# Kernel optimization log

Measured on AMD Instinct MI355X. Metric: run time of the kernel, lower is better.

## Reference

```python
import jax, jax.numpy as jnp
import numpy as np

N_NODES = 100000
NEG_SLOPE = 0.2


def gat_conv(x, W, att_src, att_dst, bias, src, dst, heads, out_ch):
    # x: [N, F_in]; W: [F_in, heads*out_ch]; att_*: [heads, out_ch]; bias: [heads*out_ch]
    N = x.shape[0]
    h = (x @ W).reshape(N, heads, out_ch)                 # [N, H, C]
    a_src = jnp.sum(h * att_src[None], axis=-1)           # [N, H]
    a_dst = jnp.sum(h * att_dst[None], axis=-1)           # [N, H]
    # per-edge unnormalized attention logits (PyG GATConv)
    alpha = jax.nn.leaky_relu(a_src[src] + a_dst[dst], NEG_SLOPE)   # [E, H]
    # scatter-softmax over edges grouped by destination node
    m = jax.ops.segment_max(alpha, dst, num_segments=N)   # [N, H]
    m = jnp.where(jnp.isfinite(m), m, 0.0)
    e = jnp.exp(alpha - m[dst])                           # [E, H]
    s = jax.ops.segment_sum(e, dst, num_segments=N)       # [N, H]
    alpha = e / (s[dst] + 1e-16)
    # weighted scatter-add aggregation of neighbor features
    out = jax.ops.segment_sum(alpha[:, :, None] * h[src], dst, num_segments=N)  # [N, H, C]
    return out.reshape(N, heads * out_ch) + bias


def setup_inputs() -> dict:
    key = jax.random.key(0)
    ks = jax.random.split(key, 10)
    F_in = 128
    x = jax.random.normal(ks[0], (N_NODES, F_in), dtype=jnp.float32)
    edge_index = jax.random.randint(ks[1], (2, 3200000), 0, N_NODES, dtype=jnp.int64)
    g = 0.1
    return {
        "x": x,
        "edge_index": edge_index,
        "W1": jax.random.normal(ks[2], (F_in, 32), jnp.float32) * g,
        "att_src1": jax.random.normal(ks[3], (2, 16), jnp.float32) * g,
        "att_dst1": jax.random.normal(ks[4], (2, 16), jnp.float32) * g,
        "b1": jnp.zeros((32,), jnp.float32),
        "W2": jax.random.normal(ks[5], (32, 2), jnp.float32) * g,
        "att_src2": jax.random.normal(ks[6], (1, 2), jnp.float32) * g,
        "att_dst2": jax.random.normal(ks[7], (1, 2), jnp.float32) * g,
        "b2": jnp.zeros((2,), jnp.float32),
    }


def reference(x, edge_index, W1, att_src1, att_dst1, b1, W2, att_src2, att_dst2, b2):
    N = x.shape[0]
    # add self-loops (PyG GATConv default add_self_loops=True)
    loops = jnp.arange(N, dtype=edge_index.dtype)
    src = jnp.concatenate([edge_index[0], loops])
    dst = jnp.concatenate([edge_index[1], loops])
    h = gat_conv(x, W1, att_src1, att_dst1, b1, src, dst, heads=2, out_ch=16)
    h = jax.nn.elu(h)
    h = gat_conv(h, W2, att_src2, att_dst2, b2, src, dst, heads=1, out_ch=2)
    return jax.nn.log_softmax(h, axis=1)
```

## Files before the change

kernel.cpp:

```cpp
#include <hip/hip_runtime.h>
#include <hip/hip_bf16.h>

#define LEAK  0.2f
#define NPB   200
#define CAP   8192
#define CAPSH 13
#define SBITS 17
#define SMASK 0x1FFFF
#define CHUNK 4096

__global__ __launch_bounds__(512) void kbin(const int* __restrict__ ei, int E, int K,
                                            int* __restrict__ cursor,
                                            int* __restrict__ binned) {
    __shared__ int hist[512], lo[512], gb[512], lc[512];
    __shared__ int2 stag[CHUNK];
    __shared__ int probe;
    int t = threadIdx.x;
    hist[t] = 0;
    if (t == 0) probe = 0;
    __syncthreads();
    if (t < 256) {
        int zc = 0;
#pragma unroll
        for (int j = 0; j < 4; j++) zc += (ei[(t * 4 + j) * 2 + 1] == 0) ? 1 : 0;
        if (zc) atomicAdd(&probe, zc);
    }
    __syncthreads();
    int f = (probe == 1024);
    int e0 = blockIdx.x * CHUNK;
    int ss[8], dd[8];
#pragma unroll
    for (int i = 0; i < 8; i++) {
        int e = e0 + t + 512 * i;
        ss[i] = -1;
        dd[i] = 0;
        if (e < E) {
            int s, d;
            if (f) { s = ei[2 * (long long)e]; d = ei[2 * ((long long)e + E)]; }
            else   { s = ei[e];                d = ei[(long long)e + E]; }
            ss[i] = s;
            dd[i] = d;
            atomicAdd(&hist[d / NPB], 1);
        }
    }
    __syncthreads();
    int v = hist[t], x = v;
    for (int o = 1; o < 512; o <<= 1) {
        int y = (t >= o) ? hist[t - o] : 0;
        __syncthreads();
        x += y;
        hist[t] = x;
        __syncthreads();
    }
    int tb = x - v;
    lo[t] = tb;
    lc[t] = tb;
    if (t < K && v) {
        int rel = atomicAdd(&cursor[t], v);
        gb[t] = (t << CAPSH) + rel;
    }
    __syncthreads();
#pragma unroll
    for (int i = 0; i < 8; i++) {
        if (ss[i] >= 0) {
            int bk = dd[i] / NPB;
            int pos = atomicAdd(&lc[bk], 1);
            stag[pos] = make_int2(ss[i], dd[i]);
        }
    }
    __syncthreads();
    int cnt = min(CHUNK, E - e0);
#pragma unroll
    for (int i = 0; i < 8; i++) {
        int idx = t + 512 * i;
        if (idx < cnt) {
            int2 sd2 = stag[idx];
            int bk = sd2.y / NPB;
            int dloc = sd2.y - bk * NPB;
            int gpos = gb[bk] + (idx - lo[bk]);
            if (gpos < ((bk + 1) << CAPSH))
                binned[gpos] = sd2.x | (dloc << SBITS);
        }
    }
}

__global__ __launch_bounds__(256) void k1(const float* __restrict__ x,
                                          const float* __restrict__ W1,
                                          const float* __restrict__ atts,
                                          const float* __restrict__ attd,
                                          float* __restrict__ h1,
                                          float* __restrict__ a1s,
                                          float* __restrict__ a1d, int N) {
    __shared__ float Ws[128 * 32];
    __shared__ float xs[64 * 132];
    int t = threadIdx.x;
    const float4* W4 = (const float4*)W1;
    float4* Ws4 = (float4*)Ws;
#pragma unroll
    for (int i = 0; i < 4; i++) Ws4[t + 256 * i] = W4[t + 256 * i];
    long long node0 = (long long)blockIdx.x * 64;
    const float4* x4 = (const float4*)x;
    float4* xs4 = (float4*)xs;
#pragma unroll
    for (int i = 0; i < 8; i++) {
        int idx = t + 256 * i;
        int row = idx >> 5, col = idx & 31;
        long long n = node0 + row;
        float4 v = make_float4(0.f, 0.f, 0.f, 0.f);
        if (n < N) v = x4[n * 32 + col];
        xs4[row * 33 + col] = v;
    }
    __syncthreads();

    int cg = t & 7, ns = t >> 3;
    const float4* xr0 = (const float4*)(xs + (ns * 2) * 132);
    const float4* xr1 = (const float4*)(xs + (ns * 2 + 1) * 132);
    float acc0[4] = {0.f, 0.f, 0.f, 0.f}, acc1[4] = {0.f, 0.f, 0.f, 0.f};
#pragma unroll 8
    for (int k4 = 0; k4 < 32; k4++) {
        float4 xa = xr0[k4], xb = xr1[k4];
        float av[4] = {xa.x, xa.y, xa.z, xa.w};
        float bv[4] = {xb.x, xb.y, xb.z, xb.w};
#pragma unroll
        for (int i = 0; i < 4; i++) {
            float4 w = Ws4[(k4 * 4 + i) * 8 + cg];
            acc0[0] = fmaf(av[i], w.x, acc0[0]);
            acc0[1] = fmaf(av[i], w.y, acc0[1]);
            acc0[2] = fmaf(av[i], w.z, acc0[2]);
            acc0[3] = fmaf(av[i], w.w, acc0[3]);
            acc1[0] = fmaf(bv[i], w.x, acc1[0]);
            acc1[1] = fmaf(bv[i], w.y, acc1[1]);
            acc1[2] = fmaf(bv[i], w.z, acc1[2]);
            acc1[3] = fmaf(bv[i], w.w, acc1[3]);
        }
    }
    long long gn0 = node0 + ns * 2, gn1 = gn0 + 1;
    float4* h14 = (float4*)h1;
    if (gn0 < N) h14[gn0 * 8 + cg] = make_float4(acc0[0], acc0[1], acc0[2], acc0[3]);
    if (gn1 < N) h14[gn1 * 8 + cg] = make_float4(acc1[0], acc1[1], acc1[2], acc1[3]);

    float ps0 = 0.f, pd0 = 0.f, ps1 = 0.f, pd1 = 0.f;
#pragma unroll
    for (int i = 0; i < 4; i++) {
        float aa = atts[cg * 4 + i], dd = attd[cg * 4 + i];
        ps0 = fmaf(acc0[i], aa, ps0);
        pd0 = fmaf(acc0[i], dd, pd0);
        ps1 = fmaf(acc1[i], aa, ps1);
        pd1 = fmaf(acc1[i], dd, pd1);
    }
#pragma unroll
    for (int m = 1; m < 4; m <<= 1) {
        ps0 += __shfl_xor(ps0, m, 64);
        pd0 += __shfl_xor(pd0, m, 64);
        ps1 += __shfl_xor(ps1, m, 64);
        pd1 += __shfl_xor(pd1, m, 64);
    }
    if ((cg & 3) == 0) {
        int hd = cg >> 2;
        if (gn0 < N) { a1s[gn0 * 2 + hd] = ps0; a1d[gn0 * 2 + hd] = pd0; }
        if (gn1 < N) { a1s[gn1 * 2 + hd] = ps1; a1d[gn1 * 2 + hd] = pd1; }
    }
}

__global__ __launch_bounds__(1024) void kfused(const int* __restrict__ cursor,
                                               const int* __restrict__ binned,
                                               const float* __restrict__ h1,
                                               const float* __restrict__ a1s,
                                               const float* __restrict__ a1d,
                                               const float* __restrict__ b1,
                                               const float* __restrict__ W2,
                                               const float* __restrict__ as2,
                                               const float* __restrict__ ad2,
                                               float4* __restrict__ pk,
                                               int* __restrict__ srcs,
                                               int* __restrict__ off,
                                               int* __restrict__ deg, int N) {
    __shared__ int lsrc[CAP];
    __shared__ int ldeg[NPB], lcur[NPB], loff[NPB];
    __shared__ int sd[1024];
    int b = blockIdx.x, t = threadIdx.x;
    int node0 = b * NPB;
    int nn = min(NPB, N - node0);
    int cnt = cursor[b];
    if (cnt > CAP) cnt = CAP;
    const int* bb = binned + ((long long)b << CAPSH);
    if (t < NPB) ldeg[t] = 0;
    __syncthreads();
    for (int i = t; i < cnt; i += 1024) atomicAdd(&ldeg[bb[i] >> SBITS], 1);
    __syncthreads();
    int v = (t < nn) ? ldeg[t] : 0, x = v;
    sd[t] = x;
    __syncthreads();
    for (int o = 1; o < 1024; o <<= 1) {
        int y = (t >= o) ? sd[t - o] : 0;
        __syncthreads();
        x += y;
        sd[t] = x;
        __syncthreads();
    }
    if (t < nn) {
        int rel = x - v;
        loff[t] = rel;
        lcur[t] = rel;
        off[node0 + t] = (b << CAPSH) + rel;
        deg[node0 + t] = v;
    }
    __syncthreads();
    for (int i = t; i < cnt; i += 1024) {
        int p = bb[i];
        int pos = atomicAdd(&lcur[p >> SBITS], 1);
        lsrc[pos] = p & SMASK;
    }
    __syncthreads();
    for (int i = t; i < cnt; i += 1024) srcs[((long long)b << CAPSH) + i] = lsrc[i];

    int wv = t >> 6, lane = t & 63;
    int e8 = lane >> 3, c4 = lane & 7, hd = c4 >> 2;
    bool wlane = (c4 & 3) == 0;
    const float4* h14 = (const float4*)h1;
    for (int ni = wv; ni < nn; ni += 16) {
        int n = node0 + ni;
        float a1dn = a1d[2 * n + hd];
        int base = loff[ni], g = ldeg[ni];
        float4 acc = make_float4(0.f, 0.f, 0.f, 0.f);
        float wsum = 0.f;
        for (int tt = e8 - 1; tt < g; tt += 8) {
            int s = (tt < 0) ? n : lsrc[base + tt];
            float al = a1s[2 * s + hd] + a1dn;
            al = al > 0.f ? al : LEAK * al;
            float w = __expf(al);
            float4 hv = h14[(size_t)s * 8 + c4];
            acc.x = fmaf(w, hv.x, acc.x);
            acc.y = fmaf(w, hv.y, acc.y);
            acc.z = fmaf(w, hv.z, acc.z);
            acc.w = fmaf(w, hv.w, acc.w);
            if (wlane) wsum += w;
        }
#pragma unroll
        for (int m = 8; m < 64; m <<= 1) {
            acc.x += __shfl_xor(acc.x, m, 64);
            acc.y += __shfl_xor(acc.y, m, 64);
            acc.z += __shfl_xor(acc.z, m, 64);
            acc.w += __shfl_xor(acc.w, m, 64);
            wsum += __shfl_xor(wsum, m, 64);
        }
        float wsH = __shfl(wsum, hd * 4, 64);
        float inv = 1.f / (wsH + 1e-16f);
        float4 bv = ((const float4*)b1)[c4];
        float4 t1;
        t1.x = acc.x * inv + bv.x;
        t1.y = acc.y * inv + bv.y;
        t1.z = acc.z * inv + bv.z;
        t1.w = acc.w * inv + bv.w;
        t1.x = t1.x > 0.f ? t1.x : __expf(t1.x) - 1.f;
        t1.y = t1.y > 0.f ? t1.y : __expf(t1.y) - 1.f;
        t1.z = t1.z > 0.f ? t1.z : __expf(t1.z) - 1.f;
        t1.w = t1.w > 0.f ? t1.w : __expf(t1.w) - 1.f;
        const float4* W24 = (const float4*)W2;
        float4 wA = W24[c4 * 2], wB = W24[c4 * 2 + 1];
        float p0 = t1.x * wA.x + t1.y * wA.z + t1.z * wB.x + t1.w * wB.z;
        float p1 = t1.x * wA.y + t1.y * wA.w + t1.z * wB.y + t1.w * wB.w;
#pragma unroll
        for (int m = 1; m < 8; m <<= 1) {
            p0 += __shfl_xor(p0, m, 64);
            p1 += __shfl_xor(p1, m, 64);
        }
        if (lane == 0)
            pk[n] = make_float4(p0 * as2[0] + p1 * as2[1], p0, p1,
                                p0 * ad2[0] + p1 * ad2[1]);
    }
}

__global__ __launch_bounds__(256) void kagg2(const int* __restrict__ off,
                                             const int* __restrict__ deg,
                                             const int* __restrict__ srcs,
                                             const float4* __restrict__ pk,
                                             const float* __restrict__ b2,
                                             float* __restrict__ out, int N) {
    int wv = threadIdx.x >> 6;
    int lane = threadIdx.x & 63;
    int n = blockIdx.x * 4 + wv;
    if (n >= N) return;
    float adn = pk[n].w;
    int base = off[n], g = deg[n];
    float a0 = 0.f, a1v = 0.f, ws = 0.f;
    for (int t = lane - 1; t < g; t += 64) {
        int s = (t < 0) ? n : srcs[base + t];
        float4 p = pk[s];
        float al = p.x + adn;
        al = al > 0.f ? al : LEAK * al;
        float w = __expf(al);
        a0 = fmaf(w, p.y, a0);
        a1v = fmaf(w, p.z, a1v);
        ws += w;
    }
#pragma unroll
    for (int m = 1; m < 64; m <<= 1) {
        a0 += __shfl_xor(a0, m, 64);
        a1v += __shfl_xor(a1v, m, 64);
        ws += __shfl_xor(ws, m, 64);
    }
    if (lane == 0) {
        float inv = 1.f / (ws + 1e-16f);
        float o0 = a0 * inv + b2[0];
        float o1 = a1v * inv + b2[1];
        float mx = fmaxf(o0, o1);
        float lse = mx + __logf(__expf(o0 - mx) + __expf(o1 - mx));
        out[2 * n] = o0 - lse;
        out[2 * n + 1] = o1 - lse;
    }
}

extern "C" void kernel_launch(void* const* d_in, const int* in_sizes, int n_in,
                              void* d_out, int out_size, void* d_ws, size_t ws_size,
                              hipStream_t stream) {
    const float* x   = (const float*)d_in[0];
    const int*   ei  = (const int*)d_in[1];
    const float* W1  = (const float*)d_in[2];
    const float* as1 = (const float*)d_in[3];
    const float* ad1 = (const float*)d_in[4];
    const float* b1  = (const float*)d_in[5];
    const float* W2  = (const float*)d_in[6];
    const float* as2 = (const float*)d_in[7];
    const float* ad2 = (const float*)d_in[8];
    const float* b2  = (const float*)d_in[9];
    float* out = (float*)d_out;

    int N = out_size / 2;
    int E = in_sizes[1] / 2;
    int K = (N + NPB - 1) / NPB;

    float* ws    = (float*)d_ws;
    float* h1    = ws;
    float4* pk   = (float4*)(h1 + (size_t)N * 32);
    float* a1s   = (float*)(pk + (size_t)N);
    float* a1d   = a1s + (size_t)N * 2;
    int* deg     = (int*)(a1d + (size_t)N * 2);
    int* off     = deg + N;
    int* srcs    = off + N;
    int* binned  = srcs + (size_t)K * CAP;
    int* cursor  = binned + (size_t)K * CAP;

    int nblkE = (E + CHUNK - 1) / CHUNK;

    hipMemsetAsync(cursor, 0, K * sizeof(int), stream);
    kbin<<<nblkE, 512, 0, stream>>>(ei, E, K, cursor, binned);
    k1<<<(N + 63) / 64, 256, 0, stream>>>(x, W1, as1, ad1, h1, a1s, a1d, N);
    kfused<<<K, 1024, 0, stream>>>(cursor, binned, h1, a1s, a1d,
                                   b1, W2, as2, ad2, pk, srcs, off, deg, N);
    kagg2<<<(N + 3) / 4, 256, 0, stream>>>(off, deg, srcs, pk, b2, out, N);
}
```

Measured before the change: 245.8 us.

## Store layer-1 features as fp16, simplify binning, pack offsets, half-wave agg2

Layer-1 hidden features are stored as packed fp16 instead of fp32, halving gather traffic in the fused aggregation. The edge binning kernel drops its shared-memory staging and block-wide scan, scattering directly with per-bucket atomics over larger chunks. The fused kernel keeps loaded edges in registers and replaces the 1024-wide shared-memory scan with a wave shuffle scan. Offset and degree are packed into one int. The second aggregation uses 32 lanes per node. The fp16 storage lowers precision, and the direct scatter writes less coalesced output.

```diff
diff --git a/kernel.cpp b/kernel.cpp
--- a/kernel.cpp
+++ b/kernel.cpp
@@ -1,19 +1,28 @@
 #include <hip/hip_runtime.h>
 #include <hip/hip_bf16.h>
-
-#define LEAK  0.2f
-#define NPB   200
-#define CAP   8192
-#define CAPSH 13
-#define SBITS 17
-#define SMASK 0x1FFFF
-#define CHUNK 4096
+#include <hip/hip_fp16.h>
+
+#define LEAK   0.2f
+#define NPB    200
+#define CAP    8192
+#define CAPSH  13
+#define SBITS  17
+#define SMASK  0x1FFFF
+#define CHUNKB 8192
+
+__device__ __forceinline__ unsigned pkh(float a, float b) {
+    __half2 h = __floats2half2_rn(a, b);
+    return *(unsigned*)&h;
+}
+__device__ __forceinline__ float2 uph(unsigned u) {
+    __half2 h = *(__half2*)&u;
+    return __half22float2(h);
+}
 
 __global__ __launch_bounds__(512) void kbin(const int* __restrict__ ei, int E, int K,
                                             int* __restrict__ cursor,
                                             int* __restrict__ binned) {
-    __shared__ int hist[512], lo[512], gb[512], lc[512];
-    __shared__ int2 stag[CHUNK];
+    __shared__ int hist[512], gb[512], lc[512];
     __shared__ int probe;
     int t = threadIdx.x;
     hist[t] = 0;
@@ -27,59 +36,36 @@
     }
     __syncthreads();
     int f = (probe == 1024);
-    int e0 = blockIdx.x * CHUNK;
-    int ss[8], dd[8];
-#pragma unroll
-    for (int i = 0; i < 8; i++) {
+    int e0 = blockIdx.x * CHUNKB;
+    int ss[16], dd[16];
+#pragma unroll
+    for (int i = 0; i < 16; i++) {
         int e = e0 + t + 512 * i;
         ss[i] = -1;
         dd[i] = 0;
         if (e < E) {
             int s, d;
-            if (f) { s = ei[2 * (long long)e]; d = ei[2 * ((long long)e + E)]; }
-            else   { s = ei[e];                d = ei[(long long)e + E]; }
+            if (f) { s = ei[2 * e]; d = ei[2 * (e + E)]; }
+            else   { s = ei[e];     d = ei[e + E]; }
             ss[i] = s;
             dd[i] = d;
             atomicAdd(&hist[d / NPB], 1);
         }
     }
     __syncthreads();
-    int v = hist[t], x = v;
-    for (int o = 1; o < 512; o <<= 1) {
-        int y = (t >= o) ? hist[t - o] : 0;
-        __syncthreads();
-        x += y;
-        hist[t] = x;
-        __syncthreads();
-    }
-    int tb = x - v;
-    lo[t] = tb;
-    lc[t] = tb;
-    if (t < K && v) {
-        int rel = atomicAdd(&cursor[t], v);
-        gb[t] = (t << CAPSH) + rel;
-    }
-    __syncthreads();
-#pragma unroll
-    for (int i = 0; i < 8; i++) {
+    int h = hist[t];
+    lc[t] = 0;
+    if (t < K && h) gb[t] = (t << CAPSH) + atomicAdd(&cursor[t], h);
+    __syncthreads();
+#pragma unroll
+    for (int i = 0; i < 16; i++) {
         if (ss[i] >= 0) {
             int bk = dd[i] / NPB;
+            int dloc = dd[i] - bk * NPB;
             int pos = atomicAdd(&lc[bk], 1);
-            stag[pos] = make_int2(ss[i], dd[i]);
-        }
-    }
-    __syncthreads();
-    int cnt = min(CHUNK, E - e0);
-#pragma unroll
-    for (int i = 0; i < 8; i++) {
-        int idx = t + 512 * i;
-        if (idx < cnt) {
-            int2 sd2 = stag[idx];
-            int bk = sd2.y / NPB;
-            int dloc = sd2.y - bk * NPB;
-            int gpos = gb[bk] + (idx - lo[bk]);
+            int gpos = gb[bk] + pos;
             if (gpos < ((bk + 1) << CAPSH))
-                binned[gpos] = sd2.x | (dloc << SBITS);
+                binned[gpos] = ss[i] | (dloc << SBITS);
         }
     }
 }
@@ -88,7 +74,7 @@
                                           const float* __restrict__ W1,
                                           const float* __restrict__ atts,
                                           const float* __restrict__ attd,
-                                          float* __restrict__ h1,
+                                          uint2* __restrict__ h1h,
                                           float* __restrict__ a1s,
                                           float* __restrict__ a1d, int N) {
     __shared__ float Ws[128 * 32];
@@ -135,9 +121,10 @@
         }
     }
     long long gn0 = node0 + ns * 2, gn1 = gn0 + 1;
-    float4* h14 = (float4*)h1;
-    if (gn0 < N) h14[gn0 * 8 + cg] = make_float4(acc0[0], acc0[1], acc0[2], acc0[3]);
-    if (gn1 < N) h14[gn1 * 8 + cg] = make_float4(acc1[0], acc1[1], acc1[2], acc1[3]);
+    if (gn0 < N) h1h[gn0 * 8 + cg] = make_uint2(pkh(acc0[0], acc0[1]),
+                                                pkh(acc0[2], acc0[3]));
+    if (gn1 < N) h1h[gn1 * 8 + cg] = make_uint2(pkh(acc1[0], acc1[1]),
+                                                pkh(acc1[2], acc1[3]));
 
     float ps0 = 0.f, pd0 = 0.f, ps1 = 0.f, pd1 = 0.f;
 #pragma unroll
@@ -164,7 +151,7 @@
 
 __global__ __launch_bounds__(1024) void kfused(const int* __restrict__ cursor,
                                                const int* __restrict__ binned,
-                                               const float* __restrict__ h1,
+                                               const uint2* __restrict__ h1h,
                                                const float* __restrict__ a1s,
                                                const float* __restrict__ a1d,
                                                const float* __restrict__ b1,
@@ -173,11 +160,10 @@
                                                const float* __restrict__ ad2,
                                                float4* __restrict__ pk,
                                                int* __restrict__ srcs,
-                                               int* __restrict__ off,
-                                               int* __restrict__ deg, int N) {
+                                               int* __restrict__ od, int N) {
     __shared__ int lsrc[CAP];
     __shared__ int ldeg[NPB], lcur[NPB], loff[NPB];
-    __shared__ int sd[1024];
+    __shared__ int swt[4];
     int b = blockIdx.x, t = threadIdx.x;
     int node0 = b * NPB;
     int nn = min(NPB, N - node0);
@@ -186,30 +172,48 @@
     const int* bb = binned + ((long long)b << CAPSH);
     if (t < NPB) ldeg[t] = 0;
     __syncthreads();
-    for (int i = t; i < cnt; i += 1024) atomicAdd(&ldeg[bb[i] >> SBITS], 1);
-    __syncthreads();
-    int v = (t < nn) ? ldeg[t] : 0, x = v;
-    sd[t] = x;
-    __syncthreads();
-    for (int o = 1; o < 1024; o <<= 1) {
-        int y = (t >= o) ? sd[t - o] : 0;
+    int pv[8];
+#pragma unroll
+    for (int j = 0; j < 8; j++) {
+        int i = t + 1024 * j;
+        pv[j] = (i < cnt) ? bb[i] : -1;
+        if (pv[j] >= 0) atomicAdd(&ldeg[pv[j] >> SBITS], 1);
+    }
+    __syncthreads();
+    {
+        int v = 0, xsc = 0;
+        if (t < 256) {
+            v = (t < nn) ? ldeg[t] : 0;
+            xsc = v;
+#pragma unroll
+            for (int o = 1; o < 64; o <<= 1) {
+                int y = __shfl_up(xsc, o, 64);
+                if ((t & 63) >= o) xsc += y;
+            }
+            if ((t & 63) == 63) swt[t >> 6] = xsc;
+        }
         __syncthreads();
-        x += y;
-        sd[t] = x;
+        if (t < 256) {
+            int add = 0;
+#pragma unroll
+            for (int j = 0; j < 4; j++)
+                if (j < (t >> 6)) add += swt[j];
+            xsc += add;
+            if (t < nn) {
+                int rel = xsc - v;
+                loff[t] = rel;
+                lcur[t] = rel;
+                od[node0 + t] = rel | (v << 14);
+            }
+        }
         __syncthreads();
     }
-    if (t < nn) {
-        int rel = x - v;
-        loff[t] = rel;
-        lcur[t] = rel;
-        off[node0 + t] = (b << CAPSH) + rel;
-        deg[node0 + t] = v;
-    }
-    __syncthreads();
-    for (int i = t; i < cnt; i += 1024) {
-        int p = bb[i];
-        int pos = atomicAdd(&lcur[p >> SBITS], 1);
-        lsrc[pos] = p & SMASK;
+#pragma unroll
+    for (int j = 0; j < 8; j++) {
+        if (pv[j] >= 0) {
+            int pos = atomicAdd(&lcur[pv[j] >> SBITS], 1);
+            lsrc[pos] = pv[j] & SMASK;
+        }
     }
     __syncthreads();
     for (int i = t; i < cnt; i += 1024) srcs[((long long)b << CAPSH) + i] = lsrc[i];
@@ -217,7 +221,6 @@
     int wv = t >> 6, lane = t & 63;
     int e8 = lane >> 3, c4 = lane & 7, hd = c4 >> 2;
     bool wlane = (c4 & 3) == 0;
-    const float4* h14 = (const float4*)h1;
     for (int ni = wv; ni < nn; ni += 16) {
         int n = node0 + ni;
         float a1dn = a1d[2 * n + hd];
@@ -229,11 +232,12 @@
             float al = a1s[2 * s + hd] + a1dn;
             al = al > 0.f ? al : LEAK * al;
             float w = __expf(al);
-            float4 hv = h14[(size_t)s * 8 + c4];
-            acc.x = fmaf(w, hv.x, acc.x);
-            acc.y = fmaf(w, hv.y, acc.y);
-            acc.z = fmaf(w, hv.z, acc.z);
-            acc.w = fmaf(w, hv.w, acc.w);
+            uint2 hb = h1h[(size_t)s * 8 + c4];
+            float2 f01 = uph(hb.x), f23 = uph(hb.y);
+            acc.x = fmaf(w, f01.x, acc.x);
+            acc.y = fmaf(w, f01.y, acc.y);
+            acc.z = fmaf(w, f23.x, acc.z);
+            acc.w = fmaf(w, f23.y, acc.w);
             if (wlane) wsum += w;
         }
 #pragma unroll
@@ -271,43 +275,42 @@
     }
 }
 
-__global__ __launch_bounds__(256) void kagg2(const int* __restrict__ off,
-                                             const int* __restrict__ deg,
+__global__ __launch_bounds__(256) void kagg2(const int* __restrict__ od,
                                              const int* __restrict__ srcs,
                                              const float4* __restrict__ pk,
                                              const float* __restrict__ b2,
                                              float* __restrict__ out, int N) {
-    int wv = threadIdx.x >> 6;
-    int lane = threadIdx.x & 63;
-    int n = blockIdx.x * 4 + wv;
+    int sub = threadIdx.x >> 5, k = threadIdx.x & 31;
+    int n = blockIdx.x * 8 + sub;
     if (n >= N) return;
-    float adn = pk[n].w;
-    int base = off[n], g = deg[n];
-    float a0 = 0.f, a1v = 0.f, ws = 0.f;
-    for (int t = lane - 1; t < g; t += 64) {
-        int s = (t < 0) ? n : srcs[base + t];
-        float4 p = pk[s];
+    float4 pn = pk[n];
+    float adn = pn.w;
+    int o = od[n];
+    int base = ((n / NPB) << CAPSH) + (o & 16383);
+    int g = o >> 14;
+    float a0 = 0.f, a1v = 0.f, wsm = 0.f;
+    for (int e = k - 1; e < g; e += 32) {
+        float4 p = (e < 0) ? pn : pk[srcs[base + e]];
         float al = p.x + adn;
         al = al > 0.f ? al : LEAK * al;
         float w = __expf(al);
         a0 = fmaf(w, p.y, a0);
         a1v = fmaf(w, p.z, a1v);
-        ws += w;
-    }
-#pragma unroll
-    for (int m = 1; m < 64; m <<= 1) {
-        a0 += __shfl_xor(a0, m, 64);
-        a1v += __shfl_xor(a1v, m, 64);
-        ws += __shfl_xor(ws, m, 64);
-    }
-    if (lane == 0) {
-        float inv = 1.f / (ws + 1e-16f);
+        wsm += w;
+    }
+#pragma unroll
+    for (int m = 1; m < 32; m <<= 1) {
+        a0 += __shfl_xor(a0, m, 32);
+        a1v += __shfl_xor(a1v, m, 32);
+        wsm += __shfl_xor(wsm, m, 32);
+    }
+    if (k == 0) {
+        float inv = 1.f / (wsm + 1e-16f);
         float o0 = a0 * inv + b2[0];
         float o1 = a1v * inv + b2[1];
         float mx = fmaxf(o0, o1);
         float lse = mx + __logf(__expf(o0 - mx) + __expf(o1 - mx));
-        out[2 * n] = o0 - lse;
-        out[2 * n + 1] = o1 - lse;
+        ((float2*)out)[n] = make_float2(o0 - lse, o1 - lse);
     }
 }
 
@@ -330,23 +333,22 @@
     int E = in_sizes[1] / 2;
     int K = (N + NPB - 1) / NPB;
 
-    float* ws    = (float*)d_ws;
-    float* h1    = ws;
-    float4* pk   = (float4*)(h1 + (size_t)N * 32);
-    float* a1s   = (float*)(pk + (size_t)N);
+    float* wsp   = (float*)d_ws;
+    float4* pk   = (float4*)wsp;
+    uint2* h1h   = (uint2*)(pk + (size_t)N);
+    float* a1s   = (float*)(h1h + (size_t)N * 8);
     float* a1d   = a1s + (size_t)N * 2;
-    int* deg     = (int*)(a1d + (size_t)N * 2);
-    int* off     = deg + N;
-    int* srcs    = off + N;
+    int* od      = (int*)(a1d + (size_t)N * 2);
+    int* srcs    = od + N;
     int* binned  = srcs + (size_t)K * CAP;
     int* cursor  = binned + (size_t)K * CAP;
 
-    int nblkE = (E + CHUNK - 1) / CHUNK;
+    int nblkB = (E + CHUNKB - 1) / CHUNKB;
 
     hipMemsetAsync(cursor, 0, K * sizeof(int), stream);
-    kbin<<<nblkE, 512, 0, stream>>>(ei, E, K, cursor, binned);
-    k1<<<(N + 63) / 64, 256, 0, stream>>>(x, W1, as1, ad1, h1, a1s, a1d, N);
-    kfused<<<K, 1024, 0, stream>>>(cursor, binned, h1, a1s, a1d,
-                                   b1, W2, as2, ad2, pk, srcs, off, deg, N);
-    kagg2<<<(N + 3) / 4, 256, 0, stream>>>(off, deg, srcs, pk, b2, out, N);
-}
+    kbin<<<nblkB, 512, 0, stream>>>(ei, E, K, cursor, binned);
+    k1<<<(N + 63) / 64, 256, 0, stream>>>(x, W1, as1, ad1, h1h, a1s, a1d, N);
+    kfused<<<K, 1024, 0, stream>>>(cursor, binned, h1h, a1s, a1d,
+                                   b1, W2, as2, ad2, pk, srcs, od, N);
+    kagg2<<<(N + 7) / 8, 256, 0, stream>>>(od, srcs, pk, b2, out, N);
+}
```

New measurement: 236.8 us. 3.7% less time.
